# Performance work log

Measured on AMD Instinct MI355X. Metric: run time of the kernel, lower is better.

Reference implementation:

```python
import jax, jax.numpy as jnp
import numpy as np

CTX = 5  # context_len

def z_vector(x, ctx):
    # x: [B, L, E] -> [B, L, ctx*E]; slot j holds embedding of token (idx + j - ctx//2), zero-padded at edges
    half = ctx // 2
    B, L, E = x.shape
    xp = jnp.pad(x, ((0, 0), (half, half), (0, 0)))
    return jnp.concatenate([xp[:, i:i + L, :] for i in range(ctx)], axis=-1)

def setup_inputs() -> dict:
    key = jax.random.key(0)
    kq, ka, kw, kb = jax.random.split(key, 4)
    B, LQ, LA, E, F = 256, 64, 256, 300, 512
    question = jax.random.normal(kq, (B, LQ, E), dtype=jnp.float32)
    answer = jax.random.normal(ka, (B, LA, E), dtype=jnp.float32)
    W = jax.random.normal(kw, (CTX * E, F), dtype=jnp.float32) * 0.02
    b = jax.random.normal(kb, (F,), dtype=jnp.float32) * 0.02
    return {"question": question, "answer": answer, "W": W, "b": b}

def reference(question, answer, W, b):
    # Conv2d(1, F, (ctx*E, 1)) over the full-height Z vector == per-position linear map
    def branch(x):
        z = z_vector(x, CTX)                       # [B, L, ctx*E]
        out = jnp.einsum('blk,kf->bfl', z, W)      # [B, F, L]
        return out + b[None, :, None]
    return branch(question), branch(answer)
```

## Files before the change

kernel.cpp:

```cpp
#include <hip/hip_runtime.h>

#define NB   256
#define E0   300
#define EP   304
#define F_   512
#define KP   1536
#define NKT  48
#define LQ_  64
#define LA_  256

typedef __attribute__((ext_vector_type(4))) float f32x4;
typedef __attribute__((ext_vector_type(8))) short short8;

#define XQ_ELEMS (NB * (LQ_ + 4) * EP)
#define XA_ELEMS (NB * (LA_ + 4) * EP)
#define WF_ELEMS (F_ * KP)
#define OUTQ_ELEMS ((size_t)NB * F_ * LQ_)
#define XROWS (NB * (LQ_ + 4) + NB * (LA_ + 4))

__device__ __forceinline__ unsigned short f2bf(float x) {
    unsigned int u = __float_as_uint(x);
    u = u + 0x7fffu + ((u >> 16) & 1u);
    return (unsigned short)(u >> 16);
}

__global__ void prep_x(const float* __restrict__ q, const float* __restrict__ a,
                       unsigned short* __restrict__ xq, unsigned short* __restrict__ xa)
{
    int idx = blockIdx.x * 256 + threadIdx.x;
    if (idx >= XROWS * 76) return;
    int row = idx / 76;
    int col = idx - row * 76;

    const float* src;
    unsigned short* dst;
    bool valid;
    if (row < NB * (LQ_ + 4)) {
        int b = row / (LQ_ + 4), lp = row - b * (LQ_ + 4);
        dst = xq + (size_t)row * EP;
        valid = (lp >= 2 && lp < 2 + LQ_);
        src = q + ((size_t)b * LQ_ + (lp - 2)) * E0;
    } else {
        int r2 = row - NB * (LQ_ + 4);
        int b = r2 / (LA_ + 4), lp = r2 - b * (LA_ + 4);
        dst = xa + (size_t)r2 * EP;
        valid = (lp >= 2 && lp < 2 + LA_);
        src = a + ((size_t)b * LA_ + (lp - 2)) * E0;
    }
    unsigned long long pk = 0ull;
    if (valid && col < 75) {
        const float4 v = reinterpret_cast<const float4*>(src)[col];
        pk = (unsigned long long)f2bf(v.x)
           | ((unsigned long long)f2bf(v.y) << 16)
           | ((unsigned long long)f2bf(v.z) << 32)
           | ((unsigned long long)f2bf(v.w) << 48);
    }
    *reinterpret_cast<unsigned long long*>(dst + (size_t)col * 4) = pk;
}

__global__ void prep_w2(const float* __restrict__ W, unsigned short* __restrict__ wfr)
{
    int idx = blockIdx.x * 256 + threadIdx.x;
    int j    = idx & 7;
    int lane = (idx >> 3) & 63;
    int chunk = idx >> 9;
    int kc = chunk % NKT;
    int tile16 = chunk / NKT;
    int f  = tile16 * 16 + (lane & 15);
    int kp = kc * 32 + (lane >> 4) * 8 + j;
    int jj = kp / EP;
    int e  = kp - jj * EP;
    float v = (kp < 5 * EP && e < E0) ? W[(size_t)(jj * E0 + e) * F_ + f] : 0.f;
    wfr[idx] = f2bf(v);
}

__global__ __launch_bounds__(256, 3) void qa_gemm(
    const unsigned short* __restrict__ xq,
    const unsigned short* __restrict__ xa,
    const unsigned short* __restrict__ wfr,
    const float* __restrict__ bias,
    float* __restrict__ out)
{
    __shared__ __align__(16) unsigned short lds[4 * 2048];

    const int bid = blockIdx.x;
    const int wg  = (bid & 7) * 320 + (bid >> 3);

    const unsigned short* xp;
    float* ob;
    int Mbase, lsh, Lp, ftBase;
    if (wg < 512) {
        Mbase  = (wg >> 1) * 64;
        ftBase = (wg & 1) * 256;
        xp = xq; lsh = 6; Lp = LQ_ + 4;
        ob = out;
    } else {
        const int id = wg - 512;
        Mbase  = (id >> 1) * 64;
        ftBase = (id & 1) * 256;
        xp = xa; lsh = 8; Lp = LA_ + 4;
        ob = out + OUTQ_ELEMS;
    }
    const int Lv = 1 << lsh;

    const int tid  = threadIdx.x;
    const int lane = tid & 63;
    const int wid  = tid >> 6;
    const int lq   = lane >> 4;
    const int lr   = lane & 15;

    const int s_c  = (lane & 3) ^ ((lane >> 3) & 3);
    const int sub  = lane >> 2;
    const int mr0 = Mbase + wid * 16 + sub;
    const unsigned short* gZ0 = xp + (size_t)((mr0 >> lsh) * Lp + (mr0 & (Lv - 1))) * EP + s_c * 8;
    const int dz0 = wid * 512;

#define GLLDS(p, d) __builtin_amdgcn_global_load_lds(                               \
        (const __attribute__((address_space(1))) void*)(p),                         \
        (__attribute__((address_space(3))) void*)(d), 16, 0, 0)
#define STAGE_Z(T) do { const int rb = ((T) & 3) * 2048; const size_t ko = (size_t)(T) * 32; \
    GLLDS(gZ0 + ko, lds + dz0 + rb); } while (0)

    const unsigned short* wpc0 = wfr + (size_t)((ftBase >> 4) + wid * 4 + 0) * NKT * 512 + lane * 8;
    const unsigned short* wpc1 = wfr + (size_t)((ftBase >> 4) + wid * 4 + 1) * NKT * 512 + lane * 8;
    const unsigned short* wpc2 = wfr + (size_t)((ftBase >> 4) + wid * 4 + 2) * NKT * 512 + lane * 8;
    const unsigned short* wpc3 = wfr + (size_t)((ftBase >> 4) + wid * 4 + 3) * NKT * 512 + lane * 8;

#define WLOAD(dst, p) do {                                                           \
    asm volatile("global_load_dwordx4 %0, %1, off" : "=v"(dst) : "v"(p) : "memory"); \
    (p) += 512; } while (0)

    const int cs = (lq ^ ((lr >> 1) & 3)) * 16;
    int zoff[4];
#pragma unroll
    for (int n = 0; n < 4; ++n) zoff[n] = (n * 16 + lr) * 64 + cs;

    f32x4 acc[4][4] = {};
    short8 WA0, WA1, WA2, WA3, WB0, WB1, WB2, WB3;

#define MFMA(a, b, c) __builtin_amdgcn_mfma_f32_16x16x32_bf16((a), (b), (c), 0, 0, 0)

#define KSTEP(T, C0, C1, C2, C3, N0, N1, N2, N3, DO_W, DO_Z, AV) do {               \
    const char* bb = (const char*)lds + ((T) & 3) * 4096;                           \
    short8 zf[4];                                                                   \
    _Pragma("unroll") for (int n = 0; n < 4; ++n) zf[n] = *(const short8*)(bb + zoff[n]); \
    if (DO_W) { WLOAD(N0, wpc0); WLOAD(N1, wpc1); WLOAD(N2, wpc2); WLOAD(N3, wpc3); } \
    if (DO_Z) { STAGE_Z((T) + 3); }                                                 \
    asm volatile("s_waitcnt vmcnt(" #AV ") lgkmcnt(0)" ::: "memory");               \
    __builtin_amdgcn_sched_barrier(0);                                              \
    _Pragma("unroll") for (int n = 0; n < 4; ++n) {                                 \
        acc[0][n] = MFMA(C0, zf[n], acc[0][n]);                                     \
        acc[1][n] = MFMA(C1, zf[n], acc[1][n]);                                     \
        acc[2][n] = MFMA(C2, zf[n], acc[2][n]);                                     \
        acc[3][n] = MFMA(C3, zf[n], acc[3][n]);                                     \
    }                                                                               \
    asm volatile("s_barrier" ::: "memory");                                         \
} while (0)

    WLOAD(WA0, wpc0); WLOAD(WA1, wpc1); WLOAD(WA2, wpc2); WLOAD(WA3, wpc3);
    STAGE_Z(0); STAGE_Z(1); STAGE_Z(2);
    asm volatile("s_waitcnt vmcnt(2)\n\ts_barrier" ::: "memory");

    for (int i = 0; i < 22; ++i) {
        const int t = 2 * i;
        KSTEP(t,     WA0, WA1, WA2, WA3, WB0, WB1, WB2, WB3, 1, 1, 6);
        KSTEP(t + 1, WB0, WB1, WB2, WB3, WA0, WA1, WA2, WA3, 1, 1, 6);
    }
    KSTEP(44, WA0, WA1, WA2, WA3, WB0, WB1, WB2, WB3, 1, 1, 6);
    KSTEP(45, WB0, WB1, WB2, WB3, WA0, WA1, WA2, WA3, 1, 0, 5);
    KSTEP(46, WA0, WA1, WA2, WA3, WB0, WB1, WB2, WB3, 1, 0, 4);
    KSTEP(47, WB0, WB1, WB2, WB3, WA0, WA1, WA2, WA3, 0, 0, 0);

#undef KSTEP
#undef WLOAD
#undef STAGE_Z
#undef GLLDS
#undef MFMA

#pragma unroll
    for (int ns = 0; ns < 4; ++ns) {
        const int m = Mbase + ns * 16 + lr;
        const int b = m >> lsh;
        const int l = m & (Lv - 1);
        float* orow = ob + ((size_t)b * F_ << lsh) + l;
#pragma unroll
        for (int ms = 0; ms < 4; ++ms) {
            const int f0 = ftBase + wid * 64 + ms * 16 + lq * 4;
            const f32x4 v = acc[ms][ns];
#pragma unroll
            for (int r = 0; r < 4; ++r)
                orow[(size_t)(f0 + r) << lsh] = v[r] + __ldg(&bias[f0 + r]);
        }
    }
}

extern "C" void kernel_launch(void* const* d_in, const int* in_sizes, int n_in,
                              void* d_out, int out_size, void* d_ws, size_t ws_size,
                              hipStream_t stream)
{
    const float* q    = (const float*)d_in[0];
    const float* a    = (const float*)d_in[1];
    const float* W    = (const float*)d_in[2];
    const float* bias = (const float*)d_in[3];
    float* out = (float*)d_out;

    unsigned short* xq  = (unsigned short*)d_ws;
    unsigned short* xa  = xq + XQ_ELEMS;
    unsigned short* wfr = xa + XA_ELEMS;

    prep_x<<<(XROWS * 76 + 255) / 256, 256, 0, stream>>>(q, a, xq, xa);
    prep_w2<<<WF_ELEMS / 256, 256, 0, stream>>>(W, wfr);
    qa_gemm<<<2560, 256, 0, stream>>>(xq, xa, wfr, bias, out);
}
```

Baseline: 169.0 us.

## Use 128-row M tiles with persistent multi-tile workgroups and deeper K staging

The GEMM tile grows from 64 to 128 rows per workgroup, so each weight fragment loaded into registers feeds twice as many MFMAs. The grid shrinks to 512 persistent workgroups that each loop over 2–3 tiles. Z is staged 128 K-elements at a time into double-buffered 64 KB LDS, and s_setprio brackets the MFMA bursts. In exchange, occupancy drops to 2 blocks per CU, register pressure rises with the 4x8 accumulator array, and the workload is split unevenly between workgroups that get 3 tiles and those that get 2.

```diff
diff --git a/kernel.cpp b/kernel.cpp
--- a/kernel.cpp
+++ b/kernel.cpp
@@ -74,124 +74,141 @@
     wfr[idx] = f2bf(v);
 }
 
-__global__ __launch_bounds__(256, 3) void qa_gemm(
+__global__ __launch_bounds__(256, 2) void qa_gemm(
     const unsigned short* __restrict__ xq,
     const unsigned short* __restrict__ xa,
     const unsigned short* __restrict__ wfr,
     const float* __restrict__ bias,
     float* __restrict__ out)
 {
-    __shared__ __align__(16) unsigned short lds[4 * 2048];
+    __shared__ __align__(16) unsigned short lds[2 * 16384];
 
     const int bid = blockIdx.x;
-    const int wg  = (bid & 7) * 320 + (bid >> 3);
-
-    const unsigned short* xp;
-    float* ob;
-    int Mbase, lsh, Lp, ftBase;
-    if (wg < 512) {
-        Mbase  = (wg >> 1) * 64;
-        ftBase = (wg & 1) * 256;
-        xp = xq; lsh = 6; Lp = LQ_ + 4;
-        ob = out;
-    } else {
-        const int id = wg - 512;
-        Mbase  = (id >> 1) * 64;
-        ftBase = (id & 1) * 256;
-        xp = xa; lsh = 8; Lp = LA_ + 4;
-        ob = out + OUTQ_ELEMS;
-    }
-    const int Lv = 1 << lsh;
+    const int wg  = (bid & 7) * 64 + (bid >> 3);
+
+    const int ftBase = (wg & 1) * 256;
+    const int ltBase = wg >> 1;
+    const int ntile  = (wg < 256) ? 3 : 2;
 
     const int tid  = threadIdx.x;
     const int lane = tid & 63;
     const int wid  = tid >> 6;
     const int lq   = lane >> 4;
     const int lr   = lane & 15;
-
     const int s_c  = (lane & 3) ^ ((lane >> 3) & 3);
     const int sub  = lane >> 2;
-    const int mr0 = Mbase + wid * 16 + sub;
-    const unsigned short* gZ0 = xp + (size_t)((mr0 >> lsh) * Lp + (mr0 & (Lv - 1))) * EP + s_c * 8;
-    const int dz0 = wid * 512;
+    const int dzA  = wid * 1024;
+    const int dzB  = dzA + 512;
+
+    const unsigned short* wb0 = wfr + (size_t)((ftBase >> 4) + wid * 4 + 0) * NKT * 512 + lane * 8;
+    const unsigned short* wb1 = wfr + (size_t)((ftBase >> 4) + wid * 4 + 1) * NKT * 512 + lane * 8;
+    const unsigned short* wb2 = wfr + (size_t)((ftBase >> 4) + wid * 4 + 2) * NKT * 512 + lane * 8;
+    const unsigned short* wb3 = wfr + (size_t)((ftBase >> 4) + wid * 4 + 3) * NKT * 512 + lane * 8;
+
+    const int cs = (lq ^ ((lr >> 1) & 3)) * 16;
+    int zoff[8];
+#pragma unroll
+    for (int n = 0; n < 8; ++n) zoff[n] = (n * 16 + lr) * 64 + cs;
 
 #define GLLDS(p, d) __builtin_amdgcn_global_load_lds(                               \
         (const __attribute__((address_space(1))) void*)(p),                         \
         (__attribute__((address_space(3))) void*)(d), 16, 0, 0)
-#define STAGE_Z(T) do { const int rb = ((T) & 3) * 2048; const size_t ko = (size_t)(T) * 32; \
-    GLLDS(gZ0 + ko, lds + dz0 + rb); } while (0)
-
-    const unsigned short* wpc0 = wfr + (size_t)((ftBase >> 4) + wid * 4 + 0) * NKT * 512 + lane * 8;
-    const unsigned short* wpc1 = wfr + (size_t)((ftBase >> 4) + wid * 4 + 1) * NKT * 512 + lane * 8;
-    const unsigned short* wpc2 = wfr + (size_t)((ftBase >> 4) + wid * 4 + 2) * NKT * 512 + lane * 8;
-    const unsigned short* wpc3 = wfr + (size_t)((ftBase >> 4) + wid * 4 + 3) * NKT * 512 + lane * 8;
-
+#define ST8(T) do { const int rb = ((T) & 1) * 16384; const size_t ko = (size_t)(T) * 128; \
+    _Pragma("unroll") for (int kb = 0; kb < 4; ++kb) {                              \
+        GLLDS(gZ0 + ko + kb * 32, lds + rb + kb * 4096 + dzA);                      \
+        GLLDS(gZ1 + ko + kb * 32, lds + rb + kb * 4096 + dzB); } } while (0)
 #define WLOAD(dst, p) do {                                                           \
     asm volatile("global_load_dwordx4 %0, %1, off" : "=v"(dst) : "v"(p) : "memory"); \
     (p) += 512; } while (0)
-
-    const int cs = (lq ^ ((lr >> 1) & 3)) * 16;
-    int zoff[4];
-#pragma unroll
-    for (int n = 0; n < 4; ++n) zoff[n] = (n * 16 + lr) * 64 + cs;
-
-    f32x4 acc[4][4] = {};
-    short8 WA0, WA1, WA2, WA3, WB0, WB1, WB2, WB3;
-
-#define MFMA(a, b, c) __builtin_amdgcn_mfma_f32_16x16x32_bf16((a), (b), (c), 0, 0, 0)
-
-#define KSTEP(T, C0, C1, C2, C3, N0, N1, N2, N3, DO_W, DO_Z, AV) do {               \
-    const char* bb = (const char*)lds + ((T) & 3) * 4096;                           \
-    short8 zf[4];                                                                   \
-    _Pragma("unroll") for (int n = 0; n < 4; ++n) zf[n] = *(const short8*)(bb + zoff[n]); \
-    if (DO_W) { WLOAD(N0, wpc0); WLOAD(N1, wpc1); WLOAD(N2, wpc2); WLOAD(N3, wpc3); } \
-    if (DO_Z) { STAGE_Z((T) + 3); }                                                 \
-    asm volatile("s_waitcnt vmcnt(" #AV ") lgkmcnt(0)" ::: "memory");               \
-    __builtin_amdgcn_sched_barrier(0);                                              \
-    _Pragma("unroll") for (int n = 0; n < 4; ++n) {                                 \
-        acc[0][n] = MFMA(C0, zf[n], acc[0][n]);                                     \
-        acc[1][n] = MFMA(C1, zf[n], acc[1][n]);                                     \
-        acc[2][n] = MFMA(C2, zf[n], acc[2][n]);                                     \
-        acc[3][n] = MFMA(C3, zf[n], acc[3][n]);                                     \
-    }                                                                               \
-    asm volatile("s_barrier" ::: "memory");                                         \
+#define W4(SET) do { WLOAD(SET[0], wp0); WLOAD(SET[1], wp1);                         \
+                     WLOAD(SET[2], wp2); WLOAD(SET[3], wp3); } while (0)
+#define ZRD4(H, KB) do { _Pragma("unroll") for (int n = 0; n < 4; ++n)               \
+    zc[(H) * 4 + n] = *(const short8*)(bbase + (KB) * 8192 + zoff[(H) * 4 + n]); } while (0)
+#define MFMA16(H, WU) do { _Pragma("unroll") for (int mf = 0; mf < 4; ++mf)          \
+    _Pragma("unroll") for (int n = 0; n < 4; ++n)                                    \
+        acc[mf][(H) * 4 + n] = __builtin_amdgcn_mfma_f32_16x16x32_bf16(              \
+            WU[mf], zc[(H) * 4 + n], acc[mf][(H) * 4 + n], 0, 0, 0); } while (0)
+#define SB __builtin_amdgcn_sched_barrier(0)
+#define KSUB(KBN, WU, WL, DO_Z, DO_W, VM) do {                                       \
+    asm volatile("s_waitcnt vmcnt(" #VM ") lgkmcnt(0)" ::: "memory"); SB;            \
+    __builtin_amdgcn_s_setprio(1); MFMA16(0, WU); __builtin_amdgcn_s_setprio(0); SB; \
+    if (DO_Z) { ZRD4(0, KBN); }                                                      \
+    __builtin_amdgcn_s_setprio(1); MFMA16(1, WU); __builtin_amdgcn_s_setprio(0); SB; \
+    if (DO_Z) { ZRD4(1, KBN); }                                                      \
+    if (DO_W) { W4(WL); }                                                            \
 } while (0)
 
-    WLOAD(WA0, wpc0); WLOAD(WA1, wpc1); WLOAD(WA2, wpc2); WLOAD(WA3, wpc3);
-    STAGE_Z(0); STAGE_Z(1); STAGE_Z(2);
-    asm volatile("s_waitcnt vmcnt(2)\n\ts_barrier" ::: "memory");
-
-    for (int i = 0; i < 22; ++i) {
-        const int t = 2 * i;
-        KSTEP(t,     WA0, WA1, WA2, WA3, WB0, WB1, WB2, WB3, 1, 1, 6);
-        KSTEP(t + 1, WB0, WB1, WB2, WB3, WA0, WA1, WA2, WA3, 1, 1, 6);
-    }
-    KSTEP(44, WA0, WA1, WA2, WA3, WB0, WB1, WB2, WB3, 1, 1, 6);
-    KSTEP(45, WB0, WB1, WB2, WB3, WA0, WA1, WA2, WA3, 1, 0, 5);
-    KSTEP(46, WA0, WA1, WA2, WA3, WB0, WB1, WB2, WB3, 1, 0, 4);
-    KSTEP(47, WB0, WB1, WB2, WB3, WA0, WA1, WA2, WA3, 0, 0, 0);
-
-#undef KSTEP
-#undef WLOAD
-#undef STAGE_Z
-#undef GLLDS
-#undef MFMA
-
-#pragma unroll
-    for (int ns = 0; ns < 4; ++ns) {
-        const int m = Mbase + ns * 16 + lr;
-        const int b = m >> lsh;
-        const int l = m & (Lv - 1);
-        float* orow = ob + ((size_t)b * F_ << lsh) + l;
-#pragma unroll
-        for (int ms = 0; ms < 4; ++ms) {
-            const int f0 = ftBase + wid * 64 + ms * 16 + lq * 4;
-            const f32x4 v = acc[ms][ns];
-#pragma unroll
-            for (int r = 0; r < 4; ++r)
-                orow[(size_t)(f0 + r) << lsh] = v[r] + __ldg(&bias[f0 + r]);
+    for (int ti = 0; ti < ntile; ++ti) {
+        const int lt = ltBase + ti * 256;
+        const unsigned short* xp;
+        float* ob;
+        int Mb, lsh, Lp;
+        if (lt < 128) { Mb = lt * 128;         xp = xq; lsh = 6; Lp = LQ_ + 4; ob = out; }
+        else          { Mb = (lt - 128) * 128; xp = xa; lsh = 8; Lp = LA_ + 4; ob = out + OUTQ_ELEMS; }
+        const int Lv = 1 << lsh;
+
+        const int mr0 = Mb + wid * 32 + sub;
+        const int mr1 = mr0 + 16;
+        const unsigned short* gZ0 = xp + (size_t)((mr0 >> lsh) * Lp + (mr0 & (Lv - 1))) * EP + s_c * 8;
+        const unsigned short* gZ1 = xp + (size_t)((mr1 >> lsh) * Lp + (mr1 & (Lv - 1))) * EP + s_c * 8;
+
+        const unsigned short* wp0 = wb0;
+        const unsigned short* wp1 = wb1;
+        const unsigned short* wp2 = wb2;
+        const unsigned short* wp3 = wb3;
+
+        f32x4 acc[4][8] = {};
+        short8 zc[8], wA[4], wB[4];
+
+        W4(wA);
+        ST8(0);
+        asm volatile("s_waitcnt vmcnt(0)\n\ts_barrier" ::: "memory");
+
+        for (int S = 0; S < 11; ++S) {
+            if (S < 11) ST8(S + 1);
+            const char* bbase = (const char*)lds + (S & 1) * 32768;
+            ZRD4(0, 0); ZRD4(1, 0);
+            KSUB(1, wA, wB, 1, 1, 8);
+            KSUB(2, wB, wA, 1, 1, 0);
+            KSUB(3, wA, wB, 1, 1, 0);
+            KSUB(0, wB, wA, 0, 1, 0);
+            asm volatile("s_barrier" ::: "memory");
+        }
+        {
+            const char* bbase = (const char*)lds + 32768;
+            ZRD4(0, 0); ZRD4(1, 0);
+            KSUB(1, wA, wB, 1, 1, 0);
+            KSUB(2, wB, wA, 1, 1, 0);
+            KSUB(3, wA, wB, 1, 1, 0);
+            KSUB(0, wB, wA, 0, 0, 0);
+            asm volatile("s_barrier" ::: "memory");
+        }
+
+#pragma unroll
+        for (int nt = 0; nt < 8; ++nt) {
+            const int m = Mb + nt * 16 + lr;
+            const int b = m >> lsh;
+            const int l = m & (Lv - 1);
+            float* orow = ob + ((size_t)b * F_ << lsh) + l;
+#pragma unroll
+            for (int mf = 0; mf < 4; ++mf) {
+                const int f0 = ftBase + wid * 64 + mf * 16 + lq * 4;
+                const f32x4 v = acc[mf][nt];
+#pragma unroll
+                for (int r = 0; r < 4; ++r)
+                    orow[(size_t)(f0 + r) << lsh] = v[r] + __ldg(&bias[f0 + r]);
+            }
         }
     }
+
+#undef KSUB
+#undef SB
+#undef MFMA16
+#undef ZRD4
+#undef W4
+#undef WLOAD
+#undef ST8
+#undef GLLDS
 }
 
 extern "C" void kernel_launch(void* const* d_in, const int* in_sizes, int n_in,
@@ -210,5 +227,5 @@
 
     prep_x<<<(XROWS * 76 + 255) / 256, 256, 0, stream>>>(q, a, xq, xa);
     prep_w2<<<WF_ELEMS / 256, 256, 0, stream>>>(W, wfr);
-    qa_gemm<<<2560, 256, 0, stream>>>(xq, xa, wfr, bias, out);
-}
+    qa_gemm<<<512, 256, 0, stream>>>(xq, xa, wfr, bias, out);
+}
```

Result: slower. 190.2 us (+12.5%).
